# Performance work log

Hardware: AMD Instinct MI355X
Metric: run time of the kernel (lower is better)

Reference implementation:

```python
import jax, jax.numpy as jnp
import numpy as np

WIDE = 15
PAD = (WIDE - 1) // 2
FREQS = np.array([1., 2., 3., 4., 5., 6.], dtype=np.float32)  # wave_base_ml frequencies


def _lstm_dir(x, wih, whh, b):
    # x: [B,T,F]; wih: [4H,F]; whh: [4H,H]; b: [4H] (b_ih+b_hh fused)
    H = whh.shape[1]
    xg = jnp.einsum('btf,gf->btg', x, wih) + b  # precompute input projections
    def step(carry, xt):
        h, c = carry
        g = xt + h @ whh.T
        i, f, gg, o = jnp.split(g, 4, axis=-1)  # torch gate order i,f,g,o
        c = jax.nn.sigmoid(f) * c + jax.nn.sigmoid(i) * jnp.tanh(gg)
        h = jax.nn.sigmoid(o) * jnp.tanh(c)
        return (h, c), h
    h0 = jnp.zeros((x.shape[0], H), x.dtype)
    _, hs = jax.lax.scan(step, (h0, h0), jnp.swapaxes(xg, 0, 1))
    return jnp.swapaxes(hs, 0, 1)


def _bn(x, g, b, eps=1e-5):
    # training-mode BatchNorm1d over (N, L) per channel; x: [B,C,L]
    m = jnp.mean(x, axis=(0, 2), keepdims=True)
    v = jnp.var(x, axis=(0, 2), keepdims=True)
    return (x - m) * jax.lax.rsqrt(v + eps) * g[None, :, None] + b[None, :, None]


def _conv1d(x, w, b):
    y = jax.lax.conv_general_dilated(x, w, (1,), 'VALID', dimension_numbers=('NCH', 'OIH', 'NCH'))
    return y + b[None, :, None]


def _haar(x):
    s = 0.7071067811865476
    return (x[..., ::2] + x[..., 1::2]) * s, (x[..., ::2] - x[..., 1::2]) * s


def _forward(x, lstm_wif, lstm_whf, lstm_bf, lstm_wir, lstm_whr, lstm_br, base_w, base_b,
             g1, be1, g2, be2, g3, be3, g4, be4, g5, be5,
             w2, b2, w3, b3, w4, b4, w5, b5, fcw, fcb):
    xt = jnp.swapaxes(x, 1, 2)  # [B,T,F]
    fwd = _lstm_dir(xt, lstm_wif, lstm_whf, lstm_bf)
    bwd = _lstm_dir(xt[:, ::-1], lstm_wir, lstm_whr, lstm_br)[:, ::-1]
    X = jnp.swapaxes(jnp.concatenate([fwd, bwd], axis=-1), 1, 2)  # [B,C,T], C=2*dim
    B, C, T = X.shape
    Xp = jnp.pad(X, ((0, 0), (0, 0), (PAD, PAD)))
    # shared sliding windows [B,C,T,WIDE] used both for scale conv and Furi_conv
    Xwin = jnp.stack([Xp[..., k:k + T] for k in range(WIDE)], axis=-1)
    offs = (jnp.arange(WIDE, dtype=X.dtype) - PAD) / WIDE
    outs = []
    for ii in range(len(FREQS)):
        scales = jax.nn.relu(jnp.einsum('bctk,k->bct', Xwin, base_w[ii]) + base_b[ii])
        # per-position cosine Fourier basis generated from the learned scales
        bases = jnp.cos((2.0 * np.pi * FREQS[ii]) * scales[..., None] * offs)  # [B,C,T,WIDE]
        o = jnp.sum(Xwin * bases, axis=-1)  # position-dependent (dynamic) conv
        sqrs = jnp.sqrt((jnp.trunc(scales * WIDE) + 1.0) / (WIDE + 2) * 2.0)
        outs.append(o / sqrs)
    wave = jnp.stack(outs, axis=1).reshape(B, -1, T)  # [B, n_waves*C, T] (wave-major, matches torch cat+view)
    out = _bn(wave, g1, be1)
    out = _bn(jax.nn.relu(_conv1d(out, w2, b2)), g2, be2)
    out = _bn(jax.nn.relu(_conv1d(out, w3, b3)), g3, be3)
    out_back = out  # [B, V_dim, L3]
    out = _bn(jax.nn.relu(_conv1d(out, w4, b4)), g4, be4)  # [B,16,L3-2]
    # 4-level Haar DWT; 5 subbands upsampled to L3, averaged over channels
    a1, d1 = _haar(out_back); a2, d2 = _haar(a1); a3, d3 = _haar(a2); a4, d4 = _haar(a3)
    L3 = out_back.shape[-1]
    bands = [jnp.repeat(bb, L3 // bb.shape[-1], axis=-1) for bb in (a4, d4, d3, d2, d1)]
    dwt = jnp.stack([bb.mean(axis=1) for bb in bands], axis=1)  # [B,5,L3]
    odwt = _bn(jax.nn.relu(_conv1d(dwt, w5, b5)), g5, be5)  # [B,16,L3-2]
    out = jnp.concatenate([out, odwt], axis=-1)
    out = out.mean(axis=-1)  # AdaptiveAvgPool1d(1) + squeeze
    return out @ fcw.T + fcb


def setup_inputs() -> dict:
    key = jax.random.key(0)
    ks = iter(jax.random.split(key, 40))
    def p(shape, s=0.05):
        return jax.random.normal(next(ks), shape, jnp.float32) * s
    B, F, T, DIM, NW, Vd = 32, 64, 518, 64, 6, 32
    C = 2 * DIM
    return {
        'x': jax.random.normal(next(ks), (B, F, T), jnp.float32),
        'lstm_wif': p((4 * DIM, F)), 'lstm_whf': p((4 * DIM, DIM)), 'lstm_bf': p((4 * DIM,)),
        'lstm_wir': p((4 * DIM, F)), 'lstm_whr': p((4 * DIM, DIM)), 'lstm_br': p((4 * DIM,)),
        'base_w': p((NW, WIDE)), 'base_b': p((NW,)),
        'g1': jnp.ones((C * NW,)), 'be1': jnp.zeros((C * NW,)),
        'g2': jnp.ones((128,)), 'be2': jnp.zeros((128,)),
        'g3': jnp.ones((Vd,)), 'be3': jnp.zeros((Vd,)),
        'g4': jnp.ones((16,)), 'be4': jnp.zeros((16,)),
        'g5': jnp.ones((16,)), 'be5': jnp.zeros((16,)),
        'w2': p((128, C * NW, 3)), 'b2': p((128,)),
        'w3': p((Vd, 128, 5)), 'b3': p((Vd,)),
        'w4': p((16, Vd, 3)), 'b4': p((16,)),
        'w5': p((16, 5, 3)), 'b5': p((16,)),
        'fcw': p((10, 16)), 'fcb': p((10,)),
    }


def reference(x, lstm_wif, lstm_whf, lstm_bf, lstm_wir, lstm_whr, lstm_br, base_w, base_b,
              g1, be1, g2, be2, g3, be3, g4, be4, g5, be5,
              w2, b2, w3, b3, w4, b4, w5, b5, fcw, fcb):
    return _forward(x, lstm_wif, lstm_whf, lstm_bf, lstm_wir, lstm_whr, lstm_br, base_w, base_b,
                    g1, be1, g2, be2, g3, be3, g4, be4, g5, be5,
                    w2, b2, w3, b3, w4, b4, w5, b5, fcw, fcb)
```

## Files before the change

### kernel.cpp

```cpp
#include <hip/hip_runtime.h>
#include <math.h>

#define B_     32
#define F_     64
#define T_     518
#define HID    64
#define GATES  256
#define CCH    128
#define NWAVE  6
#define WCH    768
#define L2_    516
#define L3_    512
#define L4_    510

typedef float v2f __attribute__((ext_vector_type(2)));

__device__ __forceinline__ float frcp(float x) { return __builtin_amdgcn_rcpf(x); }
__device__ __forceinline__ float fsigmoid(float x) { return frcp(1.f + __expf(-x)); }
__device__ __forceinline__ float ftanh(float x) { return 1.f - 2.f * frcp(1.f + __expf(2.f * x)); }

__global__ void xg_kernel(const float* __restrict__ x,
                          const float* __restrict__ wif, const float* __restrict__ bf,
                          const float* __restrict__ wir, const float* __restrict__ br,
                          float* __restrict__ xg_f, float* __restrict__ xg_r,
                          float* __restrict__ stats) {
    if (blockIdx.x == 0 && blockIdx.y == 0) {
        for (int i = threadIdx.x; i < 2 * WCH; i += 256) stats[i] = 0.f;
    }
    const int tid = threadIdx.x;
    const int g   = tid;
    const int b   = blockIdx.y;
    const int t0  = blockIdx.x * 8;
    const int sto = (g & 63) * 4 + (g >> 6);
    float4 wa[16], wb[16];
    const float4* w0 = (const float4*)(wif + g * F_);
    const float4* w1 = (const float4*)(wir + g * F_);
#pragma unroll
    for (int i = 0; i < 16; ++i) { wa[i] = w0[i]; wb[i] = w1[i]; }
    const float bfv = bf[g], brv = br[g];
    for (int tt = 0; tt < 8; ++tt) {
        const int t = t0 + tt;
        if (t >= T_) break;
        const float* xp = x + (size_t)b * F_ * T_ + t;
        float a0 = bfv, a1 = brv;
#pragma unroll
        for (int i = 0; i < 16; ++i) {
            float x0 = xp[(i * 4 + 0) * T_];
            float x1 = xp[(i * 4 + 1) * T_];
            float x2 = xp[(i * 4 + 2) * T_];
            float x3 = xp[(i * 4 + 3) * T_];
            a0 += wa[i].x * x0 + wa[i].y * x1 + wa[i].z * x2 + wa[i].w * x3;
            a1 += wb[i].x * x0 + wb[i].y * x1 + wb[i].z * x2 + wb[i].w * x3;
        }
        const size_t o = ((size_t)b * T_ + t) * GATES + sto;
        xg_f[o] = a0;
        xg_r[o] = a1;
    }
}

__global__ __attribute__((amdgpu_waves_per_eu(1, 1)))
__launch_bounds__(64) void lstm_kernel(
        const float* __restrict__ xgi_f, const float* __restrict__ xgi_r,
        const float* __restrict__ whf, const float* __restrict__ whr,
        float* __restrict__ X) {
    const int dir = blockIdx.x & 1;
    const int b   = blockIdx.x >> 1;
    const float* xg  = (dir ? xgi_r : xgi_f) + (size_t)b * T_ * GATES;
    const float* whh = dir ? whr : whf;
    const int r = threadIdx.x;

    v2f wi[32], wf[32], wg[32], wo[32];
    {
        const v2f* pI = (const v2f*)(whh + (size_t)(0 * HID + r) * HID);
        const v2f* pF = (const v2f*)(whh + (size_t)(1 * HID + r) * HID);
        const v2f* pG = (const v2f*)(whh + (size_t)(2 * HID + r) * HID);
        const v2f* pO = (const v2f*)(whh + (size_t)(3 * HID + r) * HID);
#pragma unroll
        for (int i = 0; i < 32; ++i) { wi[i] = pI[i]; wf[i] = pF[i]; wg[i] = pG[i]; wo[i] = pO[i]; }
    }

    __shared__ __align__(16) float hs[HID];
    hs[r] = 0.f;
    float c = 0.f;
    float* Xrow = X + ((size_t)(b * CCH + dir * HID + r)) * T_;

    int t = dir ? (T_ - 1) : 0;
    const int step = dir ? -1 : 1;
    const float4* xg4 = (const float4*)xg;

    int tp;
    float4 q0 = xg4[(size_t)t * HID + r];
    tp = t + step;     tp = tp < 0 ? 0 : (tp >= T_ ? T_ - 1 : tp);
    float4 q1 = xg4[(size_t)tp * HID + r];
    tp = t + 2 * step; tp = tp < 0 ? 0 : (tp >= T_ ? T_ - 1 : tp);
    float4 q2 = xg4[(size_t)tp * HID + r];
    tp = t + 3 * step; tp = tp < 0 ? 0 : (tp >= T_ ? T_ - 1 : tp);
    float4 q3 = xg4[(size_t)tp * HID + r];

    for (int s = 0; s < T_; ++s) {
        tp = t + 4 * step;
        tp = tp < 0 ? 0 : (tp >= T_ ? T_ - 1 : tp);
        const float4 qn = xg4[(size_t)tp * HID + r];

        v2f ai0 = {0.f, 0.f}, ai1 = {0.f, 0.f}, af0 = {0.f, 0.f}, af1 = {0.f, 0.f};
        v2f ag0 = {0.f, 0.f}, ag1 = {0.f, 0.f}, ao0 = {0.f, 0.f}, ao1 = {0.f, 0.f};
        const float4* h4p = (const float4*)hs;
#pragma unroll
        for (int i = 0; i < 16; ++i) {
            const float4 h4 = h4p[i];
            const v2f hlo = {h4.x, h4.y};
            const v2f hhi = {h4.z, h4.w};
            ai0 = __builtin_elementwise_fma(wi[2 * i + 0], hlo, ai0);
            ai1 = __builtin_elementwise_fma(wi[2 * i + 1], hhi, ai1);
            af0 = __builtin_elementwise_fma(wf[2 * i + 0], hlo, af0);
            af1 = __builtin_elementwise_fma(wf[2 * i + 1], hhi, af1);
            ag0 = __builtin_elementwise_fma(wg[2 * i + 0], hlo, ag0);
            ag1 = __builtin_elementwise_fma(wg[2 * i + 1], hhi, ag1);
            ao0 = __builtin_elementwise_fma(wo[2 * i + 0], hlo, ao0);
            ao1 = __builtin_elementwise_fma(wo[2 * i + 1], hhi, ao1);
        }
        const float gi  = q0.x + (ai0.x + ai0.y) + (ai1.x + ai1.y);
        const float gf  = q0.y + (af0.x + af0.y) + (af1.x + af1.y);
        const float gg_ = q0.z + (ag0.x + ag0.y) + (ag1.x + ag1.y);
        const float go  = q0.w + (ao0.x + ao0.y) + (ao1.x + ao1.y);

        const float si = fsigmoid(gi);
        const float sf = fsigmoid(gf);
        const float so = fsigmoid(go);
        c = sf * c + si * ftanh(gg_);
        const float h = so * ftanh(c);

        hs[r] = h;
        Xrow[t] = h;
        q0 = q1; q1 = q2; q2 = q3; q3 = qn;
        t += step;
    }
}

__global__ void wave_kernel(const float* __restrict__ X,
                            const float* __restrict__ bw, const float* __restrict__ bb,
                            float* __restrict__ wave, float* __restrict__ stats) {
    const int b = blockIdx.z, c = blockIdx.y;
    const int t0 = blockIdx.x * 256;
    const int tid = threadIdx.x;
    __shared__ float xs[256 + 14];
    __shared__ float bws[NWAVE][16];
    __shared__ float bbs[NWAVE];
    __shared__ float red[4][12];
    const float* xrow = X + ((size_t)(b * CCH + c)) * T_;
    for (int i = tid; i < 270; i += 256) {
        int tt = t0 - 7 + i;
        xs[i] = (tt >= 0 && tt < T_) ? xrow[tt] : 0.f;
    }
    if (tid < NWAVE * 15) bws[tid / 15][tid % 15] = bw[tid];
    if (tid < NWAVE) bbs[tid] = bb[tid];
    __syncthreads();
    const int t = t0 + tid;
    float ls[NWAVE], lq[NWAVE];
#pragma unroll
    for (int ii = 0; ii < NWAVE; ++ii) { ls[ii] = 0.f; lq[ii] = 0.f; }
    if (t < T_) {
        float win[15];
#pragma unroll
        for (int k = 0; k < 15; ++k) win[k] = xs[tid + k];
        float e[8];
        e[0] = win[7];
#pragma unroll
        for (int m = 1; m < 8; ++m) e[m] = win[7 - m] + win[7 + m];
        const float c0 = 6.28318530717958647692f / 15.f;
#pragma unroll
        for (int ii = 0; ii < NWAVE; ++ii) {
            float sc = bbs[ii];
#pragma unroll
            for (int k = 0; k < 15; ++k) sc += win[k] * bws[ii][k];
            sc = fmaxf(sc, 0.f);
            const float phi = c0 * (float)(ii + 1) * sc;
            float o = e[0];
#pragma unroll
            for (int m = 1; m < 8; ++m) o += e[m] * __cosf(phi * (float)m);
            const float q = (truncf(sc * 15.f) + 1.f) * (2.f / 17.f);
            const float val = o * rsqrtf(q);
            wave[((size_t)(b * WCH + ii * CCH + c)) * T_ + t] = val;
            ls[ii] = val;
            lq[ii] = val * val;
        }
    }
#pragma unroll
    for (int off = 32; off > 0; off >>= 1) {
#pragma unroll
        for (int ii = 0; ii < NWAVE; ++ii) {
            ls[ii] += __shfl_down(ls[ii], off);
            lq[ii] += __shfl_down(lq[ii], off);
        }
    }
    if ((tid & 63) == 0) {
        const int w = tid >> 6;
#pragma unroll
        for (int ii = 0; ii < NWAVE; ++ii) { red[w][ii] = ls[ii]; red[w][6 + ii] = lq[ii]; }
    }
    __syncthreads();
    if (tid < 12) {
        const float a = red[0][tid] + red[1][tid] + red[2][tid] + red[3][tid];
        const int ii = tid % 6;
        const int ch = ii * CCH + c;
        atomicAdd(&stats[(tid >= 6 ? WCH : 0) + ch], a);
    }
}

__global__ void bn1_finalize_kernel(const float* __restrict__ stats,
                                    float* __restrict__ mean, float* __restrict__ rstd) {
    const int c = threadIdx.x;
    const float n = (float)(B_ * T_);
    const float m = stats[c] / n;
    const float v = stats[WCH + c] / n - m * m;
    mean[c] = m;
    rstd[c] = rsqrtf(v + 1e-5f);
}

__global__ void bn_stats_kernel(const float* __restrict__ x, int Bn, int C, int L,
                                float* __restrict__ mean, float* __restrict__ rstd) {
    const int c = blockIdx.x;
    const int tid = threadIdx.x;
    float s = 0.f, s2 = 0.f;
    for (int b = 0; b < Bn; ++b) {
        const float* row = x + ((size_t)b * C + c) * L;
        for (int l = tid; l < L; l += 256) { float v = row[l]; s += v; s2 += v * v; }
    }
#pragma unroll
    for (int off = 32; off > 0; off >>= 1) { s += __shfl_down(s, off); s2 += __shfl_down(s2, off); }
    __shared__ float ss[4], ss2[4];
    if ((tid & 63) == 0) { ss[tid >> 6] = s; ss2[tid >> 6] = s2; }
    __syncthreads();
    if (tid == 0) {
        float S = ss[0] + ss[1] + ss[2] + ss[3];
        float S2 = ss2[0] + ss2[1] + ss2[2] + ss2[3];
        float n = (float)(Bn * L);
        float m = S / n;
        float v = S2 / n - m * m;
        mean[c] = m;
        rstd[c] = rsqrtf(v + 1e-5f);
    }
}

__global__ void bnfold2_kernel(const float* __restrict__ w2, const float* __restrict__ b2,
                               const float* __restrict__ m1, const float* __restrict__ r1,
                               const float* __restrict__ g1, const float* __restrict__ be1,
                               float* __restrict__ w2t, float* __restrict__ b2t) {
    const int o = blockIdx.x, tid = threadIdx.x;
    float part = 0.f;
    for (int idx = tid; idx < WCH * 3; idx += 256) {
        const int c = idx / 3;
        const float sc = r1[c] * g1[c];
        const float sh = be1[c] - m1[c] * sc;
        const float wv = w2[(size_t)o * (WCH * 3) + idx];
        w2t[(size_t)idx * 128 + o] = wv * sc;
        part += wv * sh;
    }
#pragma unroll
    for (int off = 32; off > 0; off >>= 1) part += __shfl_down(part, off);
    __shared__ float red[4];
    if ((tid & 63) == 0) red[tid >> 6] = part;
    __syncthreads();
    if (tid == 0) b2t[o] = b2[o] + red[0] + red[1] + red[2] + red[3];
}

__global__ void bnfold3_kernel(const float* __restrict__ w3, const float* __restrict__ b3,
                               const float* __restrict__ m2, const float* __restrict__ r2,
                               const float* __restrict__ g2, const float* __restrict__ be2,
                               float* __restrict__ w3t, float* __restrict__ b3t) {
    const int o = blockIdx.x, tid = threadIdx.x;
    float part = 0.f;
    for (int idx = tid; idx < 128 * 5; idx += 256) {
        const int c = idx / 5;
        const float sc = r2[c] * g2[c];
        const float sh = be2[c] - m2[c] * sc;
        const float wv = w3[(size_t)o * 640 + idx];
        w3t[(size_t)idx * 32 + o] = wv * sc;
        part += wv * sh;
    }
#pragma unroll
    for (int off = 32; off > 0; off >>= 1) part += __shfl_down(part, off);
    __shared__ float red[4];
    if ((tid & 63) == 0) red[tid >> 6] = part;
    __syncthreads();
    if (tid == 0) b3t[o] = b3[o] + red[0] + red[1] + red[2] + red[3];
}

__global__ void bnfold4_kernel(const float* __restrict__ w4, const float* __restrict__ b4,
                               const float* __restrict__ m3, const float* __restrict__ r3,
                               const float* __restrict__ g3, const float* __restrict__ be3,
                               float* __restrict__ w4t, float* __restrict__ b4t,
                               float* __restrict__ bnp3) {
    const int o = blockIdx.x, tid = threadIdx.x;
    float part = 0.f;
    if (tid < 96) {
        const int c = tid / 3;
        const float sc = r3[c] * g3[c];
        const float sh = be3[c] - m3[c] * sc;
        const float wv = w4[(size_t)o * 96 + tid];
        w4t[(size_t)tid * 16 + o] = wv * sc;
        part = wv * sh;
    }
    if (o == 0 && tid >= 96) {
        const int ch = tid - 96;
        const float sc = r3[ch] * g3[ch];
        bnp3[ch] = sc;
        bnp3[32 + ch] = be3[ch] - m3[ch] * sc;
    }
#pragma unroll
    for (int off = 32; off > 0; off >>= 1) part += __shfl_down(part, off);
    __shared__ float red[2];
    if ((tid & 63) == 0) red[tid >> 6] = part;
    __syncthreads();
    if (tid == 0) b4t[o] = b4[o] + red[0] + red[1];
}

__global__ __launch_bounds__(256) void conv2_kernel(
        const float* __restrict__ in, const float* __restrict__ wt,
        const float* __restrict__ bt, float* __restrict__ out) {
    const int b  = blockIdx.x;
    const int t  = blockIdx.y * 256 + threadIdx.x;
    const int o0 = blockIdx.z * 16;
    if (t >= L2_) return;
    v2f acc[8];
    const v2f* bt2 = (const v2f*)(bt + o0);
#pragma unroll
    for (int j = 0; j < 8; ++j) acc[j] = bt2[j];
    const float* inb = in + (size_t)b * WCH * T_ + t;
    for (int c = 0; c < WCH; ++c) {
        const float x0 = inb[c * T_], x1 = inb[c * T_ + 1], x2 = inb[c * T_ + 2];
        const v2f vx0 = {x0, x0}, vx1 = {x1, x1}, vx2 = {x2, x2};
        const v2f* wc = (const v2f*)(wt + (size_t)c * 384 + o0);
#pragma unroll
        for (int j = 0; j < 8; ++j)
            acc[j] = __builtin_elementwise_fma(wc[j], vx0,
                     __builtin_elementwise_fma(wc[64 + j], vx1,
                     __builtin_elementwise_fma(wc[128 + j], vx2, acc[j])));
    }
    const size_t ob = ((size_t)b * 128 + o0) * L2_ + t;
#pragma unroll
    for (int j = 0; j < 8; ++j) {
        out[ob + (size_t)(2 * j) * L2_]     = fmaxf(acc[j].x, 0.f);
        out[ob + (size_t)(2 * j + 1) * L2_] = fmaxf(acc[j].y, 0.f);
    }
}

__global__ __launch_bounds__(256) void conv3_kernel(
        const float* __restrict__ in, const float* __restrict__ wt,
        const float* __restrict__ bt, float* __restrict__ out) {
    const int b  = blockIdx.x;
    const int t  = blockIdx.y * 256 + threadIdx.x;
    const int o0 = blockIdx.z * 8;
    v2f acc[4];
    const v2f* bt2 = (const v2f*)(bt + o0);
#pragma unroll
    for (int j = 0; j < 4; ++j) acc[j] = bt2[j];
    const float* inb = in + (size_t)b * 128 * L2_ + t;
    for (int c = 0; c < 128; ++c) {
        const float x0 = inb[c * L2_], x1 = inb[c * L2_ + 1], x2 = inb[c * L2_ + 2];
        const float x3 = inb[c * L2_ + 3], x4 = inb[c * L2_ + 4];
        const v2f vx0 = {x0, x0}, vx1 = {x1, x1}, vx2 = {x2, x2}, vx3 = {x3, x3}, vx4 = {x4, x4};
        const v2f* wc = (const v2f*)(wt + (size_t)c * 160 + o0);
#pragma unroll
        for (int j = 0; j < 4; ++j)
            acc[j] = __builtin_elementwise_fma(wc[j], vx0,
                     __builtin_elementwise_fma(wc[16 + j], vx1,
                     __builtin_elementwise_fma(wc[32 + j], vx2,
                     __builtin_elementwise_fma(wc[48 + j], vx3,
                     __builtin_elementwise_fma(wc[64 + j], vx4, acc[j])))));
    }
    const size_t ob = ((size_t)b * 32 + o0) * L3_ + t;
#pragma unroll
    for (int j = 0; j < 4; ++j) {
        out[ob + (size_t)(2 * j) * L3_]     = fmaxf(acc[j].x, 0.f);
        out[ob + (size_t)(2 * j + 1) * L3_] = fmaxf(acc[j].y, 0.f);
    }
}

__global__ __launch_bounds__(256) void conv4_kernel(
        const float* __restrict__ in, const float* __restrict__ wt,
        const float* __restrict__ bt, float* __restrict__ out) {
    const int b = blockIdx.x;
    const int t = blockIdx.y * 256 + threadIdx.x;
    if (t >= L4_) return;
    v2f acc[8];
    const v2f* bt2 = (const v2f*)bt;
#pragma unroll
    for (int j = 0; j < 8; ++j) acc[j] = bt2[j];
    const float* inb = in + (size_t)b * 32 * L3_ + t;
    for (int c = 0; c < 32; ++c) {
        const float x0 = inb[c * L3_], x1 = inb[c * L3_ + 1], x2 = inb[c * L3_ + 2];
        const v2f vx0 = {x0, x0}, vx1 = {x1, x1}, vx2 = {x2, x2};
        const v2f* wc = (const v2f*)(wt + (size_t)c * 48);
#pragma unroll
        for (int j = 0; j < 8; ++j)
            acc[j] = __builtin_elementwise_fma(wc[j], vx0,
                     __builtin_elementwise_fma(wc[8 + j], vx1,
                     __builtin_elementwise_fma(wc[16 + j], vx2, acc[j])));
    }
    const size_t ob = ((size_t)b * 16) * L4_ + t;
#pragma unroll
    for (int j = 0; j < 8; ++j) {
        out[ob + (size_t)(2 * j) * L4_]     = fmaxf(acc[j].x, 0.f);
        out[ob + (size_t)(2 * j + 1) * L4_] = fmaxf(acc[j].y, 0.f);
    }
}

__global__ __launch_bounds__(512) void dwt_conv5_kernel(const float* __restrict__ y3,
                                                        const float* __restrict__ w5,
                                                        const float* __restrict__ b5,
                                                        const float* __restrict__ bnp3,
                                                        float* __restrict__ y5) {
    const int b = blockIdx.x, l = threadIdx.x;
    __shared__ float cm[L3_];
    __shared__ float bands[5][L3_];
    __shared__ float w5s[240];
    __shared__ float b5s[16];
    __shared__ float sc3s[32], sh3s[32];
    if (l < 240) w5s[l] = w5[l];
    if (l < 16) b5s[l] = b5[l];
    if (l >= 256 && l < 288) sc3s[l - 256] = bnp3[l - 256];
    if (l >= 288 && l < 320) sh3s[l - 288] = bnp3[32 + (l - 288)];
    __syncthreads();
    float s = 0.f, shs = 0.f;
    for (int ch = 0; ch < 32; ++ch) {
        s = fmaf(y3[((size_t)b * 32 + ch) * L3_ + l], sc3s[ch], s);
        shs += sh3s[ch];
    }
    cm[l] = (s + shs) * (1.f / 32.f);
    __syncthreads();
    const float s1 = 0.70710678118654752440f;
    const float s2c = 0.5f;
    const float s3 = 0.35355339059327378f;
    const float s4 = 0.25f;
    const int b16 = l & ~15, b8 = l & ~7, b4v = l & ~3, b2v = l & ~1;
    float sa = 0.f, sb = 0.f;
#pragma unroll
    for (int i = 0; i < 8; ++i) { sa += cm[b16 + i]; sb += cm[b16 + 8 + i]; }
    bands[0][l] = (sa + sb) * s4;
    bands[1][l] = (sa - sb) * s4;
    float ta = 0.f, tb = 0.f;
#pragma unroll
    for (int i = 0; i < 4; ++i) { ta += cm[b8 + i]; tb += cm[b8 + 4 + i]; }
    bands[2][l] = (ta - tb) * s3;
    bands[3][l] = (cm[b4v] + cm[b4v + 1] - cm[b4v + 2] - cm[b4v + 3]) * s2c;
    bands[4][l] = (cm[b2v] - cm[b2v + 1]) * s1;
    __syncthreads();
    if (l < L4_) {
        float in3[5][3];
#pragma unroll
        for (int c = 0; c < 5; ++c) {
            in3[c][0] = bands[c][l]; in3[c][1] = bands[c][l + 1]; in3[c][2] = bands[c][l + 2];
        }
#pragma unroll
        for (int o = 0; o < 16; ++o) {
            float acc = b5s[o];
#pragma unroll
            for (int c = 0; c < 5; ++c) {
                const float* wp = &w5s[(o * 5 + c) * 3];
                acc += in3[c][0] * wp[0] + in3[c][1] * wp[1] + in3[c][2] * wp[2];
            }
            y5[((size_t)b * 16 + o) * L4_ + l] = fmaxf(acc, 0.f);
        }
    }
}

__global__ __launch_bounds__(512) void tail_partial_kernel(
        const float* __restrict__ y4, const float* __restrict__ y5,
        float* __restrict__ part) {
    const int b = blockIdx.x;
    const int p = threadIdx.x;
    const int ch = p >> 5;
    const int sl = p & 31;
    const float2* p4 = (const float2*)(y4 + ((size_t)(b * 16 + ch)) * L4_);
    const float2* p5 = (const float2*)(y5 + ((size_t)(b * 16 + ch)) * L4_);
    float s4 = 0.f, q4 = 0.f, s5 = 0.f, q5 = 0.f;
    for (int i = sl; i < L4_ / 2; i += 32) {
        float2 a = p4[i], e = p5[i];
        s4 += a.x + a.y;  q4 += a.x * a.x + a.y * a.y;
        s5 += e.x + e.y;  q5 += e.x * e.x + e.y * e.y;
    }
#pragma unroll
    for (int off = 16; off > 0; off >>= 1) {
        s4 += __shfl_down(s4, off, 32); q4 += __shfl_down(q4, off, 32);
        s5 += __shfl_down(s5, off, 32); q5 += __shfl_down(q5, off, 32);
    }
    if (sl == 0) {
        float4* o = (float4*)part;
        o[b * 16 + ch] = make_float4(s4, q4, s5, q5);
    }
}

__global__ __launch_bounds__(512) void tail_final_kernel(
        const float* __restrict__ part,
        const float* __restrict__ g4, const float* __restrict__ be4,
        const float* __restrict__ g5, const float* __restrict__ be5,
        const float* __restrict__ fcw, const float* __restrict__ fcb,
        float* __restrict__ out) {
    const int p = threadIdx.x;
    const int b = p >> 4, ch = p & 15;
    const float4 v = ((const float4*)part)[b * 16 + ch];
    __shared__ float S4[512], Q4[512], S5[512], Q5[512];
    __shared__ float M4[16], R4[16], M5[16], R5[16];
    __shared__ float pool[B_][16];
    S4[p] = v.x; Q4[p] = v.y; S5[p] = v.z; Q5[p] = v.w;
    __syncthreads();
    if (p < 16) {
        float ts = 0.f, tq = 0.f, us = 0.f, uq = 0.f;
        for (int bb = 0; bb < B_; ++bb) {
            ts += S4[bb * 16 + p]; tq += Q4[bb * 16 + p];
            us += S5[bb * 16 + p]; uq += Q5[bb * 16 + p];
        }
        const float n = (float)(B_ * L4_);
        float m = ts / n; M4[p] = m; R4[p] = rsqrtf(tq / n - m * m + 1e-5f);
        m = us / n;       M5[p] = m; R5[p] = rsqrtf(uq / n - m * m + 1e-5f);
    }
    __syncthreads();
    {
        const float mm4 = v.x / (float)L4_, mm5 = v.z / (float)L4_;
        const float v4 = (mm4 - M4[ch]) * R4[ch] * g4[ch] + be4[ch];
        const float v5 = (mm5 - M5[ch]) * R5[ch] * g5[ch] + be5[ch];
        pool[b][ch] = 0.5f * (v4 + v5);
    }
    __syncthreads();
    if (p < B_ * 10) {
        const int bb = p / 10, row = p - bb * 10;
        float a = fcb[row];
#pragma unroll
        for (int c = 0; c < 16; ++c) a += pool[bb][c] * fcw[row * 16 + c];
        out[bb * 10 + row] = a;
    }
}

extern "C" void kernel_launch(void* const* d_in, const int* in_sizes, int n_in,
                              void* d_out, int out_size, void* d_ws, size_t ws_size,
                              hipStream_t stream) {
    (void)in_sizes; (void)n_in; (void)out_size; (void)ws_size;
    const float* x   = (const float*)d_in[0];
    const float* wif = (const float*)d_in[1];
    const float* whf = (const float*)d_in[2];
    const float* bf  = (const float*)d_in[3];
    const float* wir = (const float*)d_in[4];
    const float* whr = (const float*)d_in[5];
    const float* br  = (const float*)d_in[6];
    const float* bw  = (const float*)d_in[7];
    const float* bb  = (const float*)d_in[8];
    const float* g1  = (const float*)d_in[9];  const float* be1 = (const float*)d_in[10];
    const float* g2  = (const float*)d_in[11]; const float* be2 = (const float*)d_in[12];
    const float* g3  = (const float*)d_in[13]; const float* be3 = (const float*)d_in[14];
    const float* g4  = (const float*)d_in[15]; const float* be4 = (const float*)d_in[16];
    const float* g5  = (const float*)d_in[17]; const float* be5 = (const float*)d_in[18];
    const float* w2  = (const float*)d_in[19]; const float* b2  = (const float*)d_in[20];
    const float* w3  = (const float*)d_in[21]; const float* b3  = (const float*)d_in[22];
    const float* w4  = (const float*)d_in[23]; const float* b4  = (const float*)d_in[24];
    const float* w5  = (const float*)d_in[25]; const float* b5  = (const float*)d_in[26];
    const float* fcw = (const float*)d_in[27]; const float* fcb = (const float*)d_in[28];
    float* out = (float*)d_out;
    float* ws  = (float*)d_ws;

    float* xg_f  = ws;
    float* xg_r  = ws + 4243456;
    float* wave  = ws;
    float* X     = ws + 12730368;
    float* y2    = ws + 14852096;
    float* y3    = ws + 16965632;
    float* y4    = ws + 17489920;
    float* y5    = ws + 17751040;
    float* stats = ws + 18012160;
    float* m1 = ws + 18013696; float* r1 = m1 + 768;
    float* m2 = r1 + 768;      float* r2 = m2 + 128;
    float* m3 = r2 + 128;      float* r3 = m3 + 32;
    float* tpart = r3 + 32;
    float* w2t  = X;
    float* b2t  = X + 294912;
    float* w3t  = X + 295040;
    float* b3t  = X + 315520;
    float* w4t  = X + 315552;
    float* b4t  = X + 317088;
    float* bnp3 = X + 317104;

    xg_kernel<<<dim3(65, 32), 256, 0, stream>>>(x, wif, bf, wir, br, xg_f, xg_r, stats);
    lstm_kernel<<<dim3(64), 64, 0, stream>>>(xg_f, xg_r, whf, whr, X);
    wave_kernel<<<dim3(3, CCH, B_), 256, 0, stream>>>(X, bw, bb, wave, stats);
    bn1_finalize_kernel<<<dim3(1), 768, 0, stream>>>(stats, m1, r1);
    bnfold2_kernel<<<dim3(128), 256, 0, stream>>>(w2, b2, m1, r1, g1, be1, w2t, b2t);
    conv2_kernel<<<dim3(32, 3, 8), 256, 0, stream>>>(wave, w2t, b2t, y2);
    bn_stats_kernel<<<dim3(128), 256, 0, stream>>>(y2, B_, 128, L2_, m2, r2);
    bnfold3_kernel<<<dim3(32), 256, 0, stream>>>(w3, b3, m2, r2, g2, be2, w3t, b3t);
    conv3_kernel<<<dim3(32, 2, 4), 256, 0, stream>>>(y2, w3t, b3t, y3);
    bn_stats_kernel<<<dim3(32), 256, 0, stream>>>(y3, B_, 32, L3_, m3, r3);
    bnfold4_kernel<<<dim3(16), 128, 0, stream>>>(w4, b4, m3, r3, g3, be3, w4t, b4t, bnp3);
    conv4_kernel<<<dim3(32, 2), 256, 0, stream>>>(y3, w4t, b4t, y4);
    dwt_conv5_kernel<<<dim3(B_), 512, 0, stream>>>(y3, w5, b5, bnp3, y5);
    tail_partial_kernel<<<dim3(B_), 512, 0, stream>>>(y4, y5, tpart);
    tail_final_kernel<<<dim3(1), 512, 0, stream>>>(tpart, g4, be4, g5, be5, fcw, fcb, out);
}
```

Before: 1.072 ms.

## Split LSTM recurrent gates across two waves with LDS gate exchange

Result: faster. 922.7 us (-13.9%).

```diff
diff --git a/kernel.cpp b/kernel.cpp
--- a/kernel.cpp
+++ b/kernel.cpp
@@ -28,10 +28,12 @@
         for (int i = threadIdx.x; i < 2 * WCH; i += 256) stats[i] = 0.f;
     }
     const int tid = threadIdx.x;
-    const int g   = tid;
+    const int wv  = tid >> 7;
+    const int g2  = tid & 1;
+    const int r   = (tid >> 1) & 63;
+    const int g   = (2 * wv + g2) * 64 + r;
     const int b   = blockIdx.y;
     const int t0  = blockIdx.x * 8;
-    const int sto = (g & 63) * 4 + (g >> 6);
     float4 wa[16], wb[16];
     const float4* w0 = (const float4*)(wif + g * F_);
     const float4* w1 = (const float4*)(wir + g * F_);
@@ -52,14 +54,13 @@
             a0 += wa[i].x * x0 + wa[i].y * x1 + wa[i].z * x2 + wa[i].w * x3;
             a1 += wb[i].x * x0 + wb[i].y * x1 + wb[i].z * x2 + wb[i].w * x3;
         }
-        const size_t o = ((size_t)b * T_ + t) * GATES + sto;
+        const size_t o = ((size_t)b * T_ + t) * GATES + tid;
         xg_f[o] = a0;
         xg_r[o] = a1;
     }
 }
 
-__global__ __attribute__((amdgpu_waves_per_eu(1, 1)))
-__launch_bounds__(64) void lstm_kernel(
+__global__ __launch_bounds__(128, 1) void lstm_kernel(
         const float* __restrict__ xgi_f, const float* __restrict__ xgi_r,
         const float* __restrict__ whf, const float* __restrict__ whr,
         float* __restrict__ X) {
@@ -67,72 +68,64 @@
     const int b   = blockIdx.x >> 1;
     const float* xg  = (dir ? xgi_r : xgi_f) + (size_t)b * T_ * GATES;
     const float* whh = dir ? whr : whf;
-    const int r = threadIdx.x;
-
-    v2f wi[32], wf[32], wg[32], wo[32];
+    const int tid = threadIdx.x;
+    const int r   = tid & 63;
+    const int w   = tid >> 6;
+
+    float4 wA[16], wB[16];
     {
-        const v2f* pI = (const v2f*)(whh + (size_t)(0 * HID + r) * HID);
-        const v2f* pF = (const v2f*)(whh + (size_t)(1 * HID + r) * HID);
-        const v2f* pG = (const v2f*)(whh + (size_t)(2 * HID + r) * HID);
-        const v2f* pO = (const v2f*)(whh + (size_t)(3 * HID + r) * HID);
-#pragma unroll
-        for (int i = 0; i < 32; ++i) { wi[i] = pI[i]; wf[i] = pF[i]; wg[i] = pG[i]; wo[i] = pO[i]; }
-    }
-
-    __shared__ __align__(16) float hs[HID];
-    hs[r] = 0.f;
+        const float4* pA = (const float4*)(whh + (size_t)((2 * w) * HID + r) * HID);
+        const float4* pB = (const float4*)(whh + (size_t)((2 * w + 1) * HID + r) * HID);
+#pragma unroll
+        for (int i = 0; i < 16; ++i) { wA[i] = pA[i]; wB[i] = pB[i]; }
+    }
+
+    __shared__ __align__(16) float hs[2][HID];
+    __shared__ __align__(16) float gbuf[2][HID][4];
+    hs[w][r] = 0.f;
     float c = 0.f;
     float* Xrow = X + ((size_t)(b * CCH + dir * HID + r)) * T_;
 
     int t = dir ? (T_ - 1) : 0;
     const int step = dir ? -1 : 1;
-    const float4* xg4 = (const float4*)xg;
-
-    int tp;
-    float4 q0 = xg4[(size_t)t * HID + r];
-    tp = t + step;     tp = tp < 0 ? 0 : (tp >= T_ ? T_ - 1 : tp);
-    float4 q1 = xg4[(size_t)tp * HID + r];
-    tp = t + 2 * step; tp = tp < 0 ? 0 : (tp >= T_ ? T_ - 1 : tp);
-    float4 q2 = xg4[(size_t)tp * HID + r];
-    tp = t + 3 * step; tp = tp < 0 ? 0 : (tp >= T_ ? T_ - 1 : tp);
-    float4 q3 = xg4[(size_t)tp * HID + r];
+    const float2* xg2 = (const float2*)xg;
+    float2 q0 = xg2[((size_t)t * 2 + w) * 64 + r];
+    float2 q1 = xg2[((size_t)(t + step) * 2 + w) * 64 + r];
 
     for (int s = 0; s < T_; ++s) {
-        tp = t + 4 * step;
-        tp = tp < 0 ? 0 : (tp >= T_ ? T_ - 1 : tp);
-        const float4 qn = xg4[(size_t)tp * HID + r];
-
-        v2f ai0 = {0.f, 0.f}, ai1 = {0.f, 0.f}, af0 = {0.f, 0.f}, af1 = {0.f, 0.f};
-        v2f ag0 = {0.f, 0.f}, ag1 = {0.f, 0.f}, ao0 = {0.f, 0.f}, ao1 = {0.f, 0.f};
-        const float4* h4p = (const float4*)hs;
+        float4 a0 = {q0.x, 0.f, 0.f, 0.f};
+        float4 a1 = {q0.y, 0.f, 0.f, 0.f};
+        const float4* h4p = (const float4*)hs[w];
 #pragma unroll
         for (int i = 0; i < 16; ++i) {
             const float4 h4 = h4p[i];
-            const v2f hlo = {h4.x, h4.y};
-            const v2f hhi = {h4.z, h4.w};
-            ai0 = __builtin_elementwise_fma(wi[2 * i + 0], hlo, ai0);
-            ai1 = __builtin_elementwise_fma(wi[2 * i + 1], hhi, ai1);
-            af0 = __builtin_elementwise_fma(wf[2 * i + 0], hlo, af0);
-            af1 = __builtin_elementwise_fma(wf[2 * i + 1], hhi, af1);
-            ag0 = __builtin_elementwise_fma(wg[2 * i + 0], hlo, ag0);
-            ag1 = __builtin_elementwise_fma(wg[2 * i + 1], hhi, ag1);
-            ao0 = __builtin_elementwise_fma(wo[2 * i + 0], hlo, ao0);
-            ao1 = __builtin_elementwise_fma(wo[2 * i + 1], hhi, ao1);
-        }
-        const float gi  = q0.x + (ai0.x + ai0.y) + (ai1.x + ai1.y);
-        const float gf  = q0.y + (af0.x + af0.y) + (af1.x + af1.y);
-        const float gg_ = q0.z + (ag0.x + ag0.y) + (ag1.x + ag1.y);
-        const float go  = q0.w + (ao0.x + ao0.y) + (ao1.x + ao1.y);
-
-        const float si = fsigmoid(gi);
-        const float sf = fsigmoid(gf);
-        const float so = fsigmoid(go);
-        c = sf * c + si * ftanh(gg_);
+            a0.x = fmaf(wA[i].x, h4.x, a0.x); a0.y = fmaf(wA[i].y, h4.y, a0.y);
+            a0.z = fmaf(wA[i].z, h4.z, a0.z); a0.w = fmaf(wA[i].w, h4.w, a0.w);
+            a1.x = fmaf(wB[i].x, h4.x, a1.x); a1.y = fmaf(wB[i].y, h4.y, a1.y);
+            a1.z = fmaf(wB[i].z, h4.z, a1.z); a1.w = fmaf(wB[i].w, h4.w, a1.w);
+        }
+        const float gA = (a0.x + a0.y) + (a0.z + a0.w);
+        const float gB = (a1.x + a1.y) + (a1.z + a1.w);
+        const int buf = s & 1;
+        *(float2*)&gbuf[buf][r][2 * w] = make_float2(gA, gB);
+
+        int tp = t + 2 * step;
+        tp = tp < 0 ? 0 : (tp >= T_ ? T_ - 1 : tp);
+        const float2 qn = xg2[((size_t)tp * 2 + w) * 64 + r];
+
+        asm volatile("s_waitcnt lgkmcnt(0)" ::: "memory");
+        __builtin_amdgcn_s_barrier();
+
+        const float4 g4 = *(const float4*)gbuf[buf][r];
+        const float si = fsigmoid(g4.x);
+        const float sf = fsigmoid(g4.y);
+        const float so = fsigmoid(g4.w);
+        c = sf * c + si * ftanh(g4.z);
         const float h = so * ftanh(c);
 
-        hs[r] = h;
-        Xrow[t] = h;
-        q0 = q1; q1 = q2; q2 = q3; q3 = qn;
+        hs[w][r] = h;
+        if (w == 0) Xrow[t] = h;
+        q0 = q1; q1 = qn;
         t += step;
     }
 }
@@ -580,7 +573,7 @@
     float* bnp3 = X + 317104;
 
     xg_kernel<<<dim3(65, 32), 256, 0, stream>>>(x, wif, bf, wir, br, xg_f, xg_r, stats);
-    lstm_kernel<<<dim3(64), 64, 0, stream>>>(xg_f, xg_r, whf, whr, X);
+    lstm_kernel<<<dim3(64), 128, 0, stream>>>(xg_f, xg_r, whf, whr, X);
     wave_kernel<<<dim3(3, CCH, B_), 256, 0, stream>>>(X, bw, bb, wave, stats);
     bn1_finalize_kernel<<<dim3(1), 768, 0, stream>>>(stats, m1, r1);
     bnfold2_kernel<<<dim3(128), 256, 0, stream>>>(w2, b2, m1, r1, g1, be1, w2t, b2t);
```
